# Optimization experiments

Measured on AMD Instinct MI355X. Metric: run time of the kernel, lower is better.

Reference implementation:

```python
import jax, jax.numpy as jnp
import numpy as np

B, S, D = 4, 2048, 768
H = 12
HD = D // H
SCALE = HD ** -0.5


def setup_inputs() -> dict:
    key = jax.random.key(0)
    ks = jax.random.split(key, 5)
    std = D ** -0.5
    return {
        "hidden_states": jax.random.normal(ks[0], (B, S, D), dtype=jnp.float32),
        "qkv_w": jax.random.normal(ks[1], (3 * D, D), dtype=jnp.float32) * std,
        "qkv_b": jnp.zeros((3 * D,), dtype=jnp.float32),
        "proj_w": jax.random.normal(ks[2], (D, D), dtype=jnp.float32) * std,
        "proj_b": jnp.zeros((D,), dtype=jnp.float32),
    }


def reference(hidden_states, qkv_w, qkv_b, proj_w, proj_b):
    b, s, d = hidden_states.shape
    # fused QKV projection: [b,s,3d] -> [3,b,H,s,hd]
    mixed = hidden_states @ qkv_w.T + qkv_b
    mixed = mixed.reshape(b, s, 3, H, HD).transpose(2, 0, 3, 1, 4)
    q, k, v = mixed[0], mixed[1], mixed[2]
    # naive attention: full [b,H,s,s] score matrix, as in original module
    scores = jnp.einsum("bhqd,bhkd->bhqk", q, k) * SCALE
    probs = jax.nn.softmax(scores, axis=-1)
    ctx = jnp.einsum("bhqk,bhkd->bhqd", probs, v)
    ctx = ctx.transpose(0, 2, 1, 3).reshape(b, s, d)
    out = ctx @ proj_w.T + proj_b
    return out
```

## Files before the change

### kernel.cpp

```cpp
#include <hip/hip_runtime.h>
#include <hip/hip_bf16.h>

using short8   = __attribute__((ext_vector_type(8))) short;
using floatx4  = __attribute__((ext_vector_type(4))) float;
using floatx16 = __attribute__((ext_vector_type(16))) float;

#define KDIM 768
#define QSCALE 0.18033688011112042f

__device__ __forceinline__ short f2bf(float f) {
    union { float f; unsigned u; } v; v.f = f;
    unsigned r = v.u + 0x7fffu + ((v.u >> 16) & 1u);
    return (short)(r >> 16);
}

__device__ __forceinline__ unsigned pack2bf(float a, float b) {
    __hip_bfloat162 h = __float22bfloat162_rn(float2{a, b});
    union { __hip_bfloat162 h; unsigned u; } c; c.h = h;
    return c.u;
}

__device__ __forceinline__ float fast_exp2(float x) {
#if __has_builtin(__builtin_amdgcn_exp2f)
    return __builtin_amdgcn_exp2f(x);
#else
    return exp2f(x);
#endif
}

__device__ __forceinline__ void async16(const void* g, void* l) {
    __builtin_amdgcn_global_load_lds((const __attribute__((address_space(1))) void*)g,
                                     (__attribute__((address_space(3))) void*)l, 16, 0, 0);
}

__global__ void cvt_f32_bf16(const float* __restrict__ in, short* __restrict__ out, int n) {
    int i = (blockIdx.x * blockDim.x + threadIdx.x) * 4;
    if (i >= n) return;
    float4 v = *(const float4*)(in + i);
    short4 o;
    o.x = f2bf(v.x); o.y = f2bf(v.y); o.z = f2bf(v.z); o.w = f2bf(v.w);
    *(short4*)(out + i) = o;
}

__global__ __launch_bounds__(256) void gemm_qkv(
    const short* __restrict__ X, const short* __restrict__ W,
    const float* __restrict__ bias,
    short* __restrict__ Qb, short* __restrict__ Kb, short* __restrict__ Vb)
{
    __shared__ short As[128 * 32];
    __shared__ short Bs[128 * 32];
    int tid = threadIdx.x;
    int w = tid >> 6, l = tid & 63;
    int lane16 = l & 15, quad = l >> 4;
    int wm = w & 1, wn = w >> 1;
    int m0 = blockIdx.y * 128, n0 = blockIdx.x * 128;

    floatx4 acc[4][4] = {};

    int srow = w * 32 + (l >> 2);
    int scol = (l & 3) * 8;
    const short* Xg = X + (size_t)(m0 + srow) * KDIM + scol;
    const short* Wg = W + (size_t)(n0 + srow) * KDIM + scol;
    short* AsW = As + (w * 32) * 32;
    short* BsW = Bs + (w * 32) * 32;

    for (int kb = 0; kb < KDIM; kb += 32) {
        __syncthreads();
        async16(Xg + kb,              AsW);
        async16(Xg + kb + 16 * KDIM,  AsW + 16 * 32);
        async16(Wg + kb,              BsW);
        async16(Wg + kb + 16 * KDIM,  BsW + 16 * 32);
        __syncthreads();
        short8 a[4], b[4];
#pragma unroll
        for (int mt = 0; mt < 4; mt++) a[mt] = *(const short8*)(As + (wm * 64 + mt * 16 + lane16) * 32 + quad * 8);
#pragma unroll
        for (int nt = 0; nt < 4; nt++) b[nt] = *(const short8*)(Bs + (wn * 64 + nt * 16 + lane16) * 32 + quad * 8);
#pragma unroll
        for (int mt = 0; mt < 4; mt++)
#pragma unroll
            for (int nt = 0; nt < 4; nt++)
                acc[mt][nt] = __builtin_amdgcn_mfma_f32_16x16x32_bf16(a[mt], b[nt], acc[mt][nt], 0, 0, 0);
    }

#pragma unroll
    for (int mt = 0; mt < 4; mt++) {
        int row = m0 + wm * 64 + mt * 16 + quad * 4;
#pragma unroll
        for (int nt = 0; nt < 4; nt++) {
            int col = n0 + wn * 64 + nt * 16 + lane16;
            int qkv = (col >= 1536) ? 2 : ((col >= 768) ? 1 : 0);
            int rem = col - qkv * 768;
            int h = rem >> 6, e = rem & 63;
            short* dst = (qkv == 0) ? Qb : ((qkv == 1) ? Kb : Vb);
            float sc = (qkv == 0) ? (float)QSCALE : 1.0f;
            float bv = bias[col];
#pragma unroll
            for (int r = 0; r < 4; r++) {
                int i  = row + r;
                int b_ = i >> 11, s_ = i & 2047;
                dst[(((size_t)(b_ * 12 + h)) * 2048 + s_) * 64 + e] = f2bf((acc[mt][nt][r] + bv) * sc);
            }
        }
    }
}

__global__ __launch_bounds__(256) void transpose_v(
    const short* __restrict__ Vb, short* __restrict__ Vt)
{
    __shared__ short T[64 * 66];
    int tid = threadIdx.x;
    int s0 = blockIdx.x * 64, bh = blockIdx.y;
    const short* src = Vb + (size_t)bh * 2048 * 64;
    short* dst = Vt + (size_t)bh * 64 * 2048;

#pragma unroll
    for (int i = 0; i < 2; i++) {
        int slot = i * 256 + tid;
        int s_loc = slot >> 3, ec = slot & 7;
        short8 v = *(const short8*)(src + (size_t)(s0 + s_loc) * 64 + ec * 8);
        *(short8*)(T + s_loc * 66 + ec * 8) = v;
    }
    __syncthreads();
#pragma unroll
    for (int i = 0; i < 2; i++) {
        int slot = i * 256 + tid;
        int e_loc = slot >> 3, sc = slot & 7;
        short8 o;
#pragma unroll
        for (int j = 0; j < 8; j++) o[j] = T[(sc * 8 + j) * 66 + e_loc];
        *(short8*)(dst + (size_t)e_loc * 2048 + s0 + sc * 8) = o;
    }
}

__global__ __launch_bounds__(256, 3) void attn(
    const short* __restrict__ Qb, const short* __restrict__ Kb,
    const short* __restrict__ Vt, short* __restrict__ Ctx)
{
    __shared__ short Ks[512 * 8];
    __shared__ short Vs[512 * 8];
    __shared__ short Ps[4][256 * 8];
    int tid = threadIdx.x, w = tid >> 6, l = tid & 63;
    int l32 = l & 31, half = l >> 5;
    int qt = blockIdx.x, bh = blockIdx.y;
    const short* Qh  = Qb + (size_t)bh * 2048 * 64;
    const short* Kh  = Kb + (size_t)bh * 2048 * 64;
    const short* Vth = Vt + (size_t)bh * 64 * 2048;
    int qbase = qt * 128 + w * 32;
    short* Psw = &Ps[w][0];

    const short* kSrc[2];
    const short* vSrc[2];
    short* kDst[2];
    short* vDst[2];
#pragma unroll
    for (int i = 0; i < 2; i++) {
        int slot = i * 256 + tid;
        int row = slot >> 3;
        int g = (slot & 7) ^ (row & 7);
        kSrc[i] = Kh + (size_t)row * 64 + g * 8;
        vSrc[i] = Vth + (size_t)row * 2048 + g * 8;
        kDst[i] = Ks + (size_t)(i * 256 + w * 64) * 8;
        vDst[i] = Vs + (size_t)(i * 256 + w * 64) * 8;
    }

    short8 qf[4];
#pragma unroll
    for (int ks = 0; ks < 4; ks++)
        qf[ks] = *(const short8*)(Qh + (size_t)(qbase + l32) * 64 + ks * 16 + half * 8);

    float lsum[16];
#pragma unroll
    for (int r = 0; r < 16; r++) lsum[r] = 0.f;
    floatx16 acc[2] = {};

    for (int kt = 0; kt < 32; kt++) {
        __syncthreads();
#pragma unroll
        for (int i = 0; i < 2; i++) {
            async16(kSrc[i] + (size_t)kt * 64 * 64, kDst[i]);
            async16(vSrc[i] + (size_t)kt * 64,      vDst[i]);
        }
        __syncthreads();

        floatx16 s[2];
#pragma unroll
        for (int nt = 0; nt < 2; nt++) {
            floatx16 c = {};
#pragma unroll
            for (int ks = 0; ks < 4; ks++) {
                int row = nt * 32 + l32;
                int chunk = ks * 2 + half;
                short8 kf = *(const short8*)(Ks + (size_t)(row * 8 + (chunk ^ (row & 7))) * 8);
                c = __builtin_amdgcn_mfma_f32_32x32x16_bf16(qf[ks], kf, c, 0, 0, 0);
            }
            s[nt] = c;
        }

#pragma unroll
        for (int nt = 0; nt < 2; nt++) {
            int key = nt * 32 + l32;
            int chunk = key >> 3, pos = key & 7;
#pragma unroll
            for (int r = 0; r < 16; r += 2) {
                float p0 = fast_exp2(s[nt][r]);
                float p1 = fast_exp2(s[nt][r + 1]);
                lsum[r]     += p0;
                lsum[r + 1] += p1;
                int row0 = (r & 3) + 8 * (r >> 2) + 4 * half;
                unsigned pk = pack2bf(p0, p1);
                Psw[(size_t)(row0 * 8 + (chunk ^ (row0 & 7))) * 8 + pos]       = (short)(pk & 0xffff);
                Psw[(size_t)((row0 + 1) * 8 + (chunk ^ ((row0 + 1) & 7))) * 8 + pos] = (short)(pk >> 16);
            }
        }

        short8 pa[4];
#pragma unroll
        for (int ks = 0; ks < 4; ks++) {
            int chunk = ks * 2 + half;
            pa[ks] = *(const short8*)(Psw + (size_t)(l32 * 8 + (chunk ^ (l32 & 7))) * 8);
        }
#pragma unroll
        for (int nt = 0; nt < 2; nt++) {
#pragma unroll
            for (int ks = 0; ks < 4; ks++) {
                int row = nt * 32 + l32;
                int chunk = ks * 2 + half;
                short8 vf = *(const short8*)(Vs + (size_t)(row * 8 + (chunk ^ (row & 7))) * 8);
                acc[nt] = __builtin_amdgcn_mfma_f32_32x32x16_bf16(pa[ks], vf, acc[nt], 0, 0, 0);
            }
        }
    }

    float inv[16];
#pragma unroll
    for (int r = 0; r < 16; r++) {
        float t = lsum[r];
        t += __shfl_xor(t, 1);
        t += __shfl_xor(t, 2);
        t += __shfl_xor(t, 4);
        t += __shfl_xor(t, 8);
        t += __shfl_xor(t, 16);
        inv[r] = 1.0f / t;
    }
    int b_ = bh / 12, h = bh % 12;
#pragma unroll
    for (int nt = 0; nt < 2; nt++)
#pragma unroll
        for (int r = 0; r < 16; r++) {
            int q = qbase + (r & 3) + 8 * (r >> 2) + 4 * half;
            int e = nt * 32 + l32;
            Ctx[((size_t)(b_ * 2048 + q)) * 768 + h * 64 + e] = f2bf(acc[nt][r] * inv[r]);
        }
}

__global__ __launch_bounds__(256) void gemm_out(
    const short* __restrict__ Ctx, const short* __restrict__ W,
    const float* __restrict__ bias, float* __restrict__ out)
{
    __shared__ short As[128 * 32];
    __shared__ short Bs[128 * 32];
    int tid = threadIdx.x;
    int w = tid >> 6, l = tid & 63;
    int lane16 = l & 15, quad = l >> 4;
    int wm = w & 1, wn = w >> 1;
    int m0 = blockIdx.y * 128, n0 = blockIdx.x * 128;

    floatx4 acc[4][4] = {};

    int srow = w * 32 + (l >> 2);
    int scol = (l & 3) * 8;
    const short* Xg = Ctx + (size_t)(m0 + srow) * KDIM + scol;
    const short* Wg = W + (size_t)(n0 + srow) * KDIM + scol;
    short* AsW = As + (w * 32) * 32;
    short* BsW = Bs + (w * 32) * 32;

    for (int kb = 0; kb < KDIM; kb += 32) {
        __syncthreads();
        async16(Xg + kb,             AsW);
        async16(Xg + kb + 16 * KDIM, AsW + 16 * 32);
        async16(Wg + kb,             BsW);
        async16(Wg + kb + 16 * KDIM, BsW + 16 * 32);
        __syncthreads();
        short8 a[4], b[4];
#pragma unroll
        for (int mt = 0; mt < 4; mt++) a[mt] = *(const short8*)(As + (wm * 64 + mt * 16 + lane16) * 32 + quad * 8);
#pragma unroll
        for (int nt = 0; nt < 4; nt++) b[nt] = *(const short8*)(Bs + (wn * 64 + nt * 16 + lane16) * 32 + quad * 8);
#pragma unroll
        for (int mt = 0; mt < 4; mt++)
#pragma unroll
            for (int nt = 0; nt < 4; nt++)
                acc[mt][nt] = __builtin_amdgcn_mfma_f32_16x16x32_bf16(a[mt], b[nt], acc[mt][nt], 0, 0, 0);
    }

#pragma unroll
    for (int mt = 0; mt < 4; mt++) {
        int row = m0 + wm * 64 + mt * 16 + quad * 4;
#pragma unroll
        for (int nt = 0; nt < 4; nt++) {
            int col = n0 + wn * 64 + nt * 16 + lane16;
            float bv = bias[col];
#pragma unroll
            for (int r = 0; r < 4; r++)
                out[(size_t)(row + r) * 768 + col] = acc[mt][nt][r] + bv;
        }
    }
}

extern "C" void kernel_launch(void* const* d_in, const int* in_sizes, int n_in,
                              void* d_out, int out_size, void* d_ws, size_t ws_size,
                              hipStream_t stream) {
    const float* hs     = (const float*)d_in[0];
    const float* qkv_w  = (const float*)d_in[1];
    const float* qkv_b  = (const float*)d_in[2];
    const float* proj_w = (const float*)d_in[3];
    const float* proj_b = (const float*)d_in[4];
    float* out = (float*)d_out;

    short* Xb  = (short*)d_ws;
    short* W1b = Xb  + (size_t)8192 * 768;
    short* W2b = W1b + (size_t)2304 * 768;
    short* Qb  = W2b + (size_t)768 * 768;
    short* Kb  = Qb  + (size_t)8192 * 768;
    short* Vb  = Kb  + (size_t)8192 * 768;
    short* Ctx = Vb  + (size_t)8192 * 768;
    short* Vt  = Xb;

    int n1 = 8192 * 768;
    cvt_f32_bf16<<<n1 / 4 / 256, 256, 0, stream>>>(hs, Xb, n1);
    int n2 = 2304 * 768;
    cvt_f32_bf16<<<n2 / 4 / 256, 256, 0, stream>>>(qkv_w, W1b, n2);
    int n3 = 768 * 768;
    cvt_f32_bf16<<<n3 / 4 / 256, 256, 0, stream>>>(proj_w, W2b, n3);

    gemm_qkv<<<dim3(18, 64), 256, 0, stream>>>(Xb, W1b, qkv_b, Qb, Kb, Vb);
    transpose_v<<<dim3(32, 48), 256, 0, stream>>>(Vb, Vt);
    attn<<<dim3(16, 48), 256, 0, stream>>>(Qb, Kb, Vt, Ctx);
    gemm_out<<<dim3(6, 64), 256, 0, stream>>>(Ctx, W2b, proj_b, out);
}
```

Measured before the change: 238.6 us.

## Restructure attention to 2 waves with 64 query rows each, fuse conversion kernels

The attention kernel now runs 128 threads per block, and each wave handles two 32-row query blocks. K and V fragments are loaded from LDS once and reused across both blocks, which halves LDS fragment traffic per MFMA. The V transpose permutes key order so each lane can write its two exp'd probabilities as one packed 32-bit store into the P buffer, instead of two 16-bit scattered stores. The three fp32→bf16 conversion launches are merged into one kernel to cut launch overhead, at the cost of higher register pressure and fewer waves per block in attention.

Result: slower. 249.8 us (+4.7%).

```diff
diff --git a/kernel.cpp b/kernel.cpp
--- a/kernel.cpp
+++ b/kernel.cpp
@@ -7,6 +7,9 @@
 
 #define KDIM 768
 #define QSCALE 0.18033688011112042f
+#define N1 (8192 * 768)
+#define N2 (2304 * 768)
+#define N3 (768 * 768)
 
 __device__ __forceinline__ short f2bf(float f) {
     union { float f; unsigned u; } v; v.f = f;
@@ -33,13 +36,19 @@
                                      (__attribute__((address_space(3))) void*)l, 16, 0, 0);
 }
 
-__global__ void cvt_f32_bf16(const float* __restrict__ in, short* __restrict__ out, int n) {
+__global__ void cvt_all(const float* __restrict__ a, const float* __restrict__ b,
+                        const float* __restrict__ c, short* __restrict__ oa,
+                        short* __restrict__ ob, short* __restrict__ oc) {
     int i = (blockIdx.x * blockDim.x + threadIdx.x) * 4;
-    if (i >= n) return;
-    float4 v = *(const float4*)(in + i);
+    const float* src; short* dst;
+    if (i < N1)            { src = a + i;            dst = oa + i; }
+    else if (i < N1 + N2)  { src = b + (i - N1);     dst = ob + (i - N1); }
+    else if (i < N1+N2+N3) { src = c + (i - N1 - N2); dst = oc + (i - N1 - N2); }
+    else return;
+    float4 v = *(const float4*)src;
     short4 o;
     o.x = f2bf(v.x); o.y = f2bf(v.y); o.z = f2bf(v.z); o.w = f2bf(v.w);
-    *(short4*)(out + i) = o;
+    *(short4*)dst = o;
 }
 
 __global__ __launch_bounds__(256) void gemm_qkv(
@@ -128,130 +137,148 @@
         int e_loc = slot >> 3, sc = slot & 7;
         short8 o;
 #pragma unroll
-        for (int j = 0; j < 8; j++) o[j] = T[(sc * 8 + j) * 66 + e_loc];
+        for (int j = 0; j < 8; j++) {
+            int p = sc * 8 + j;
+            int kp = (p >> 1) + (p & 1) * 32;
+            o[j] = T[kp * 66 + e_loc];
+        }
         *(short8*)(dst + (size_t)e_loc * 2048 + s0 + sc * 8) = o;
     }
 }
 
-__global__ __launch_bounds__(256, 3) void attn(
+__global__ __launch_bounds__(128, 2) void attn(
     const short* __restrict__ Qb, const short* __restrict__ Kb,
     const short* __restrict__ Vt, short* __restrict__ Ctx)
 {
     __shared__ short Ks[512 * 8];
     __shared__ short Vs[512 * 8];
-    __shared__ short Ps[4][256 * 8];
+    __shared__ short Ps[2][512 * 8];
     int tid = threadIdx.x, w = tid >> 6, l = tid & 63;
     int l32 = l & 31, half = l >> 5;
     int qt = blockIdx.x, bh = blockIdx.y;
     const short* Qh  = Qb + (size_t)bh * 2048 * 64;
     const short* Kh  = Kb + (size_t)bh * 2048 * 64;
     const short* Vth = Vt + (size_t)bh * 64 * 2048;
-    int qbase = qt * 128 + w * 32;
+    int qbase = qt * 128 + w * 64;
     short* Psw = &Ps[w][0];
 
-    const short* kSrc[2];
-    const short* vSrc[2];
-    short* kDst[2];
-    short* vDst[2];
-#pragma unroll
-    for (int i = 0; i < 2; i++) {
-        int slot = i * 256 + tid;
+    const short* kSrc[4];
+    const short* vSrc[4];
+    short* kDst[4];
+    short* vDst[4];
+#pragma unroll
+    for (int i = 0; i < 4; i++) {
+        int slot = w * 256 + i * 64 + l;
         int row = slot >> 3;
         int g = (slot & 7) ^ (row & 7);
         kSrc[i] = Kh + (size_t)row * 64 + g * 8;
         vSrc[i] = Vth + (size_t)row * 2048 + g * 8;
-        kDst[i] = Ks + (size_t)(i * 256 + w * 64) * 8;
-        vDst[i] = Vs + (size_t)(i * 256 + w * 64) * 8;
-    }
-
-    short8 qf[4];
-#pragma unroll
-    for (int ks = 0; ks < 4; ks++)
-        qf[ks] = *(const short8*)(Qh + (size_t)(qbase + l32) * 64 + ks * 16 + half * 8);
-
-    float lsum[16];
-#pragma unroll
-    for (int r = 0; r < 16; r++) lsum[r] = 0.f;
-    floatx16 acc[2] = {};
+        kDst[i] = Ks + (size_t)(w * 256 + i * 64) * 8;
+        vDst[i] = Vs + (size_t)(w * 256 + i * 64) * 8;
+    }
+
+    short8 qf[2][4];
+#pragma unroll
+    for (int mb = 0; mb < 2; mb++)
+#pragma unroll
+        for (int ks = 0; ks < 4; ks++)
+            qf[mb][ks] = *(const short8*)(Qh + (size_t)(qbase + mb * 32 + l32) * 64 + ks * 16 + half * 8);
+
+    float lsum[2][16];
+#pragma unroll
+    for (int mb = 0; mb < 2; mb++)
+#pragma unroll
+        for (int r = 0; r < 16; r++) lsum[mb][r] = 0.f;
+    floatx16 acc[2][2] = {};
 
     for (int kt = 0; kt < 32; kt++) {
         __syncthreads();
 #pragma unroll
-        for (int i = 0; i < 2; i++) {
+        for (int i = 0; i < 4; i++) {
             async16(kSrc[i] + (size_t)kt * 64 * 64, kDst[i]);
             async16(vSrc[i] + (size_t)kt * 64,      vDst[i]);
         }
         __syncthreads();
 
-        floatx16 s[2];
-#pragma unroll
-        for (int nt = 0; nt < 2; nt++) {
-            floatx16 c = {};
+        short8 kf[2][4];
+#pragma unroll
+        for (int nt = 0; nt < 2; nt++)
 #pragma unroll
             for (int ks = 0; ks < 4; ks++) {
                 int row = nt * 32 + l32;
                 int chunk = ks * 2 + half;
-                short8 kf = *(const short8*)(Ks + (size_t)(row * 8 + (chunk ^ (row & 7))) * 8);
-                c = __builtin_amdgcn_mfma_f32_32x32x16_bf16(qf[ks], kf, c, 0, 0, 0);
-            }
-            s[nt] = c;
-        }
-
-#pragma unroll
-        for (int nt = 0; nt < 2; nt++) {
-            int key = nt * 32 + l32;
-            int chunk = key >> 3, pos = key & 7;
-#pragma unroll
-            for (int r = 0; r < 16; r += 2) {
-                float p0 = fast_exp2(s[nt][r]);
-                float p1 = fast_exp2(s[nt][r + 1]);
-                lsum[r]     += p0;
-                lsum[r + 1] += p1;
-                int row0 = (r & 3) + 8 * (r >> 2) + 4 * half;
-                unsigned pk = pack2bf(p0, p1);
-                Psw[(size_t)(row0 * 8 + (chunk ^ (row0 & 7))) * 8 + pos]       = (short)(pk & 0xffff);
-                Psw[(size_t)((row0 + 1) * 8 + (chunk ^ ((row0 + 1) & 7))) * 8 + pos] = (short)(pk >> 16);
-            }
-        }
-
-        short8 pa[4];
-#pragma unroll
-        for (int ks = 0; ks < 4; ks++) {
-            int chunk = ks * 2 + half;
-            pa[ks] = *(const short8*)(Psw + (size_t)(l32 * 8 + (chunk ^ (l32 & 7))) * 8);
-        }
-#pragma unroll
-        for (int nt = 0; nt < 2; nt++) {
+                kf[nt][ks] = *(const short8*)(Ks + (size_t)(row * 8 + (chunk ^ (row & 7))) * 8);
+            }
+
+#pragma unroll
+        for (int mb = 0; mb < 2; mb++) {
+            floatx16 s0 = {}, s1 = {};
+#pragma unroll
+            for (int ks = 0; ks < 4; ks++) {
+                s0 = __builtin_amdgcn_mfma_f32_32x32x16_bf16(qf[mb][ks], kf[0][ks], s0, 0, 0, 0);
+                s1 = __builtin_amdgcn_mfma_f32_32x32x16_bf16(qf[mb][ks], kf[1][ks], s1, 0, 0, 0);
+            }
+#pragma unroll
+            for (int r = 0; r < 16; r++) {
+                float p0 = fast_exp2(s0[r]);
+                float p1 = fast_exp2(s1[r]);
+                lsum[mb][r] += p0 + p1;
+                int q = mb * 32 + (r & 3) + 8 * (r >> 2) + 4 * half;
+                int slot = q * 8 + ((l32 >> 2) ^ (q & 7));
+                *(unsigned*)&Psw[slot * 8 + (l32 & 3) * 2] = pack2bf(p0, p1);
+            }
+        }
+
+        short8 vf[2][4];
+#pragma unroll
+        for (int nt = 0; nt < 2; nt++)
 #pragma unroll
             for (int ks = 0; ks < 4; ks++) {
                 int row = nt * 32 + l32;
                 int chunk = ks * 2 + half;
-                short8 vf = *(const short8*)(Vs + (size_t)(row * 8 + (chunk ^ (row & 7))) * 8);
-                acc[nt] = __builtin_amdgcn_mfma_f32_32x32x16_bf16(pa[ks], vf, acc[nt], 0, 0, 0);
-            }
-        }
-    }
-
-    float inv[16];
-#pragma unroll
-    for (int r = 0; r < 16; r++) {
-        float t = lsum[r];
-        t += __shfl_xor(t, 1);
-        t += __shfl_xor(t, 2);
-        t += __shfl_xor(t, 4);
-        t += __shfl_xor(t, 8);
-        t += __shfl_xor(t, 16);
-        inv[r] = 1.0f / t;
-    }
+                vf[nt][ks] = *(const short8*)(Vs + (size_t)(row * 8 + (chunk ^ (row & 7))) * 8);
+            }
+#pragma unroll
+        for (int mb = 0; mb < 2; mb++) {
+            short8 pa[4];
+#pragma unroll
+            for (int ks = 0; ks < 4; ks++) {
+                int row = mb * 32 + l32;
+                int chunk = ks * 2 + half;
+                pa[ks] = *(const short8*)(Psw + (size_t)(row * 8 + (chunk ^ (row & 7))) * 8);
+            }
+#pragma unroll
+            for (int nt = 0; nt < 2; nt++)
+#pragma unroll
+                for (int ks = 0; ks < 4; ks++)
+                    acc[mb][nt] = __builtin_amdgcn_mfma_f32_32x32x16_bf16(pa[ks], vf[nt][ks], acc[mb][nt], 0, 0, 0);
+        }
+    }
+
+    float inv[2][16];
+#pragma unroll
+    for (int mb = 0; mb < 2; mb++)
+#pragma unroll
+        for (int r = 0; r < 16; r++) {
+            float t = lsum[mb][r];
+            t += __shfl_xor(t, 1);
+            t += __shfl_xor(t, 2);
+            t += __shfl_xor(t, 4);
+            t += __shfl_xor(t, 8);
+            t += __shfl_xor(t, 16);
+            inv[mb][r] = 1.0f / t;
+        }
     int b_ = bh / 12, h = bh % 12;
 #pragma unroll
-    for (int nt = 0; nt < 2; nt++)
-#pragma unroll
-        for (int r = 0; r < 16; r++) {
-            int q = qbase + (r & 3) + 8 * (r >> 2) + 4 * half;
-            int e = nt * 32 + l32;
-            Ctx[((size_t)(b_ * 2048 + q)) * 768 + h * 64 + e] = f2bf(acc[nt][r] * inv[r]);
-        }
+    for (int mb = 0; mb < 2; mb++)
+#pragma unroll
+        for (int nt = 0; nt < 2; nt++)
+#pragma unroll
+            for (int r = 0; r < 16; r++) {
+                int q = qbase + mb * 32 + (r & 3) + 8 * (r >> 2) + 4 * half;
+                int e = nt * 32 + l32;
+                Ctx[((size_t)(b_ * 2048 + q)) * 768 + h * 64 + e] = f2bf(acc[mb][nt][r] * inv[mb][r]);
+            }
 }
 
 __global__ __launch_bounds__(256) void gemm_out(
@@ -327,15 +354,11 @@
     short* Ctx = Vb  + (size_t)8192 * 768;
     short* Vt  = Xb;
 
-    int n1 = 8192 * 768;
-    cvt_f32_bf16<<<n1 / 4 / 256, 256, 0, stream>>>(hs, Xb, n1);
-    int n2 = 2304 * 768;
-    cvt_f32_bf16<<<n2 / 4 / 256, 256, 0, stream>>>(qkv_w, W1b, n2);
-    int n3 = 768 * 768;
-    cvt_f32_bf16<<<n3 / 4 / 256, 256, 0, stream>>>(proj_w, W2b, n3);
+    int ntot = (N1 + N2 + N3) / 4;
+    cvt_all<<<(ntot + 255) / 256, 256, 0, stream>>>(hs, qkv_w, proj_w, Xb, W1b, W2b);
 
     gemm_qkv<<<dim3(18, 64), 256, 0, stream>>>(Xb, W1b, qkv_b, Qb, Kb, Vb);
     transpose_v<<<dim3(32, 48), 256, 0, stream>>>(Vb, Vt);
-    attn<<<dim3(16, 48), 256, 0, stream>>>(Qb, Kb, Vt, Ctx);
+    attn<<<dim3(16, 48), 128, 0, stream>>>(Qb, Kb, Vt, Ctx);
     gemm_out<<<dim3(6, 64), 256, 0, stream>>>(Ctx, W2b, proj_b, out);
 }
```

## Load K fragments directly from global, pack P pairs, and fuse conversion kernels

Applied to the files above, without the earlier changes.

The attention kernel no longer stages K tiles through shared memory. Each lane reads its K fragment straight from global memory, which removes the K async copies and the LDS reads. Score columns are paired across the two 32-key subtiles so two exp results pack into one 32-bit LDS store. To keep the PV product consistent, the key order inside Vt is permuted in transpose_v. The three fp32-to-bf16 conversion launches are merged into one kernel to cut launch overhead. The risk is that uncached global K loads add latency on the critical MFMA path.

Result: slower. 275.0 us (+15.3%).

```diff
diff --git a/kernel.cpp b/kernel.cpp
--- a/kernel.cpp
+++ b/kernel.cpp
@@ -7,6 +7,9 @@
 
 #define KDIM 768
 #define QSCALE 0.18033688011112042f
+#define N1 (8192 * 768)
+#define N2 (2304 * 768)
+#define N3 (768 * 768)
 
 __device__ __forceinline__ short f2bf(float f) {
     union { float f; unsigned u; } v; v.f = f;
@@ -33,13 +36,19 @@
                                      (__attribute__((address_space(3))) void*)l, 16, 0, 0);
 }
 
-__global__ void cvt_f32_bf16(const float* __restrict__ in, short* __restrict__ out, int n) {
+__global__ void cvt_all(const float* __restrict__ a, const float* __restrict__ b,
+                        const float* __restrict__ c, short* __restrict__ oa,
+                        short* __restrict__ ob, short* __restrict__ oc) {
     int i = (blockIdx.x * blockDim.x + threadIdx.x) * 4;
-    if (i >= n) return;
-    float4 v = *(const float4*)(in + i);
+    const float* src; short* dst;
+    if (i < N1)            { src = a + i;            dst = oa + i; }
+    else if (i < N1 + N2)  { src = b + (i - N1);     dst = ob + (i - N1); }
+    else if (i < N1+N2+N3) { src = c + (i - N1 - N2); dst = oc + (i - N1 - N2); }
+    else return;
+    float4 v = *(const float4*)src;
     short4 o;
     o.x = f2bf(v.x); o.y = f2bf(v.y); o.z = f2bf(v.z); o.w = f2bf(v.w);
-    *(short4*)(out + i) = o;
+    *(short4*)dst = o;
 }
 
 __global__ __launch_bounds__(256) void gemm_qkv(
@@ -128,7 +137,11 @@
         int e_loc = slot >> 3, sc = slot & 7;
         short8 o;
 #pragma unroll
-        for (int j = 0; j < 8; j++) o[j] = T[(sc * 8 + j) * 66 + e_loc];
+        for (int j = 0; j < 8; j++) {
+            int p = sc * 8 + j;
+            int kp = (p >> 1) + (p & 1) * 32;
+            o[j] = T[kp * 66 + e_loc];
+        }
         *(short8*)(dst + (size_t)e_loc * 2048 + s0 + sc * 8) = o;
     }
 }
@@ -137,7 +150,6 @@
     const short* __restrict__ Qb, const short* __restrict__ Kb,
     const short* __restrict__ Vt, short* __restrict__ Ctx)
 {
-    __shared__ short Ks[512 * 8];
     __shared__ short Vs[512 * 8];
     __shared__ short Ps[4][256 * 8];
     int tid = threadIdx.x, w = tid >> 6, l = tid & 63;
@@ -149,18 +161,14 @@
     int qbase = qt * 128 + w * 32;
     short* Psw = &Ps[w][0];
 
-    const short* kSrc[2];
     const short* vSrc[2];
-    short* kDst[2];
     short* vDst[2];
 #pragma unroll
     for (int i = 0; i < 2; i++) {
         int slot = i * 256 + tid;
         int row = slot >> 3;
         int g = (slot & 7) ^ (row & 7);
-        kSrc[i] = Kh + (size_t)row * 64 + g * 8;
         vSrc[i] = Vth + (size_t)row * 2048 + g * 8;
-        kDst[i] = Ks + (size_t)(i * 256 + w * 64) * 8;
         vDst[i] = Vs + (size_t)(i * 256 + w * 64) * 8;
     }
 
@@ -177,41 +185,33 @@
     for (int kt = 0; kt < 32; kt++) {
         __syncthreads();
 #pragma unroll
-        for (int i = 0; i < 2; i++) {
-            async16(kSrc[i] + (size_t)kt * 64 * 64, kDst[i]);
-            async16(vSrc[i] + (size_t)kt * 64,      vDst[i]);
-        }
-        __syncthreads();
-
-        floatx16 s[2];
-#pragma unroll
-        for (int nt = 0; nt < 2; nt++) {
-            floatx16 c = {};
+        for (int i = 0; i < 2; i++)
+            async16(vSrc[i] + (size_t)kt * 64, vDst[i]);
+        __syncthreads();
+
+        floatx16 s0 = {}, s1 = {};
+        {
+            const short* kbase = Kh + (size_t)kt * 64 * 64;
 #pragma unroll
             for (int ks = 0; ks < 4; ks++) {
-                int row = nt * 32 + l32;
-                int chunk = ks * 2 + half;
-                short8 kf = *(const short8*)(Ks + (size_t)(row * 8 + (chunk ^ (row & 7))) * 8);
-                c = __builtin_amdgcn_mfma_f32_32x32x16_bf16(qf[ks], kf, c, 0, 0, 0);
+                short8 kf = *(const short8*)(kbase + (size_t)l32 * 64 + ks * 16 + half * 8);
+                s0 = __builtin_amdgcn_mfma_f32_32x32x16_bf16(qf[ks], kf, s0, 0, 0, 0);
             }
-            s[nt] = c;
-        }
-
-#pragma unroll
-        for (int nt = 0; nt < 2; nt++) {
-            int key = nt * 32 + l32;
-            int chunk = key >> 3, pos = key & 7;
-#pragma unroll
-            for (int r = 0; r < 16; r += 2) {
-                float p0 = fast_exp2(s[nt][r]);
-                float p1 = fast_exp2(s[nt][r + 1]);
-                lsum[r]     += p0;
-                lsum[r + 1] += p1;
-                int row0 = (r & 3) + 8 * (r >> 2) + 4 * half;
-                unsigned pk = pack2bf(p0, p1);
-                Psw[(size_t)(row0 * 8 + (chunk ^ (row0 & 7))) * 8 + pos]       = (short)(pk & 0xffff);
-                Psw[(size_t)((row0 + 1) * 8 + (chunk ^ ((row0 + 1) & 7))) * 8 + pos] = (short)(pk >> 16);
+#pragma unroll
+            for (int ks = 0; ks < 4; ks++) {
+                short8 kf = *(const short8*)(kbase + (size_t)(32 + l32) * 64 + ks * 16 + half * 8);
+                s1 = __builtin_amdgcn_mfma_f32_32x32x16_bf16(qf[ks], kf, s1, 0, 0, 0);
             }
+        }
+
+#pragma unroll
+        for (int r = 0; r < 16; r++) {
+            float p0 = fast_exp2(s0[r]);
+            float p1 = fast_exp2(s1[r]);
+            lsum[r] += p0 + p1;
+            int q = (r & 3) + 8 * (r >> 2) + 4 * half;
+            int slot = q * 8 + ((l32 >> 2) ^ (q & 7));
+            *(unsigned*)&Psw[slot * 8 + (l32 & 3) * 2] = pack2bf(p0, p1);
         }
 
         short8 pa[4];
@@ -327,12 +327,8 @@
     short* Ctx = Vb  + (size_t)8192 * 768;
     short* Vt  = Xb;
 
-    int n1 = 8192 * 768;
-    cvt_f32_bf16<<<n1 / 4 / 256, 256, 0, stream>>>(hs, Xb, n1);
-    int n2 = 2304 * 768;
-    cvt_f32_bf16<<<n2 / 4 / 256, 256, 0, stream>>>(qkv_w, W1b, n2);
-    int n3 = 768 * 768;
-    cvt_f32_bf16<<<n3 / 4 / 256, 256, 0, stream>>>(proj_w, W2b, n3);
+    int ntot = (N1 + N2 + N3) / 4;
+    cvt_all<<<(ntot + 255) / 256, 256, 0, stream>>>(hs, qkv_w, proj_w, Xb, W1b, W2b);
 
     gemm_qkv<<<dim3(18, 64), 256, 0, stream>>>(Xb, W1b, qkv_b, Qb, Kb, Vb);
     transpose_v<<<dim3(32, 48), 256, 0, stream>>>(Vb, Vt);
```
